# Kernel tuning notes

Measured on AMD Instinct MI355X. Metric: run time of the kernel, lower is better.

## Reference

```python
import jax, jax.numpy as jnp
import numpy as np

EPS = 1e-5  # torch GroupNorm default eps


def _pairwise_sqdist(x, y):
    # squared euclidean distance matrix, clamped at 0 for numerical safety
    d = (jnp.sum(x * x, -1)[:, None] + jnp.sum(y * y, -1)[None, :]
         - 2.0 * (x @ y.T))
    return jnp.maximum(d, 0.0)


def _pc_normalize(ref, src):
    # jointly center and scale both clouds to the unit sphere
    pts = jnp.concatenate([ref, src], axis=0)
    centroid = pts.mean(axis=0, keepdims=True)
    pts = pts - centroid
    m = jnp.max(jnp.linalg.norm(pts, axis=1))
    pts = pts / m
    n_ref = ref.shape[0]
    return pts[:n_ref], pts[n_ref:]


def _group_norm(x, gamma, beta, groups):
    N, C = x.shape
    xg = x.reshape(N, groups, C // groups)
    mean = xg.mean(-1, keepdims=True)
    var = jnp.mean((xg - mean) ** 2, -1, keepdims=True)
    xn = ((xg - mean) / jnp.sqrt(var + EPS)).reshape(N, C)
    return xn * gamma + beta


def setup_inputs() -> dict:
    key = jax.random.key(0)
    ks = jax.random.split(key, 8)
    N_ref, N_src, D = 128, 128, 256
    points_c = jax.random.normal(ks[0], (N_ref + N_src, 3), jnp.float32)
    ref_feats = jax.random.normal(ks[1], (N_ref, D), jnp.float32)
    src_feats = jax.random.normal(ks[2], (N_src, D), jnp.float32)
    # normalized features, as the '_norm' names suggest
    ref_feats = ref_feats / jnp.linalg.norm(ref_feats, axis=-1, keepdims=True)
    src_feats = src_feats / jnp.linalg.norm(src_feats, axis=-1, keepdims=True)
    # a valid rigid transform: random rotation + small translation
    A = jax.random.normal(ks[3], (3, 3), jnp.float32)
    Q, _ = jnp.linalg.qr(A)
    trans = jnp.eye(4, dtype=jnp.float32)
    trans = trans.at[:3, :3].set(Q)
    trans = trans.at[:3, 3].set(jax.random.normal(ks[4], (3,), jnp.float32) * 0.1)
    s = 1.0 / np.sqrt(512)
    return {
        'points_c': points_c,
        'ref_feats_c_norm': ref_feats,
        'src_feats_c_norm': src_feats,
        'trans': trans,
        'W1': jax.random.normal(ks[5], (256, 512), jnp.float32) * s,
        'b1': jnp.zeros((256,), jnp.float32),
        'g1': jnp.ones((256,), jnp.float32),
        'bt1': jnp.zeros((256,), jnp.float32),
        'W2': jax.random.normal(ks[6], (128, 256), jnp.float32) * (1.0 / np.sqrt(256)),
        'b2': jnp.zeros((128,), jnp.float32),
        'g2': jnp.ones((128,), jnp.float32),
        'bt2': jnp.zeros((128,), jnp.float32),
        'W3': jax.random.normal(ks[7], (2, 128), jnp.float32) * (1.0 / np.sqrt(128)),
        'b3': jnp.zeros((2,), jnp.float32),
        'ref_length': 128,
    }


def reference(points_c, ref_feats_c_norm, src_feats_c_norm, trans,
              W1, b1, g1, bt1, W2, b2, g2, bt2, W3, b3, ref_length):
    GROUPS = 8
    ref_points = points_c[:ref_length]
    src_points = points_c[ref_length:]
    # apply rigid transform to src points
    src_points = src_points @ trans[:3, :3].T + trans[:3, 3]
    ref_n, src_n = _pc_normalize(ref_points, src_points)

    dist_mat = jnp.exp(-_pairwise_sqdist(ref_n, src_n))  # [Nr, Ns]
    match_idx_ref = jnp.argmax(dist_mat, axis=1)
    match_idx_src = jnp.argmax(dist_mat, axis=0)
    min_dist_ref = jnp.max(dist_mat, axis=1)
    min_dist_src = jnp.max(dist_mat, axis=0)

    feat_score_mat = ref_feats_c_norm @ src_feats_c_norm.T  # [Nr, Ns]
    feat_match_idx_ref = jnp.argmax(feat_score_mat, axis=1)
    feat_match_idx_src = jnp.argmax(feat_score_mat, axis=0)
    feat_match_ref = jnp.max(feat_score_mat, axis=1)
    feat_match_src = jnp.max(feat_score_mat, axis=0)

    r_idx = jnp.arange(feat_score_mat.shape[0])
    c_idx = jnp.arange(feat_score_mat.shape[1])
    feat_score_ref = feat_score_mat[r_idx, match_idx_ref]
    feat_score_src = feat_score_mat[match_idx_src, c_idx]
    dist_ref = dist_mat[r_idx, feat_match_idx_ref]
    dist_src = dist_mat[feat_match_idx_src, c_idx]

    min_dist = jnp.concatenate([min_dist_ref, min_dist_src])
    feat_score = jnp.concatenate([feat_score_ref, feat_score_src])
    perm_d = jnp.argsort(-min_dist)  # descending sort
    d_m = min_dist[perm_d] * feat_score[perm_d]

    match_feat = jnp.concatenate([feat_match_ref, feat_match_src])
    match_dist = jnp.concatenate([dist_ref, dist_src])
    perm_f = jnp.argsort(-match_feat)
    m_d = match_dist[perm_f] * match_feat[perm_f]

    geo_out = jnp.concatenate([d_m, m_d])[None, :]  # [1, 512]

    h = _group_norm(geo_out @ W1.T + b1, g1, bt1, GROUPS)
    h = jax.nn.relu(h)
    h = _group_norm(h @ W2.T + b2, g2, bt2, GROUPS)
    h = jax.nn.relu(h)
    return h @ W3.T + b3  # [1, num_classes]
```

## Files before the change

kernel.cpp:

```cpp
#include <hip/hip_runtime.h>
#include <math.h>

#define NREF 128
#define NSRC 128
#define DIM  256
#define EPS  1e-5f

__global__ __launch_bounds__(512) void feat_kernel(
    const float* __restrict__ ref_feats,
    const float* __restrict__ src_feats,
    float* __restrict__ feat_mat)
{
    __shared__ __align__(16) float refrow[DIM];
    const int i = blockIdx.x;
    const int t = threadIdx.x;
    if (t < 64) ((float4*)refrow)[t] = ((const float4*)(ref_feats + i * DIM))[t];
    __syncthreads();

    const int w = t >> 6, l = t & 63;
    const float4 r = ((const float4*)refrow)[l];

    for (int m = 0; m < 16; m += 2) {
        const int j0 = w * 16 + m;
        const int j1 = j0 + 1;
        const float4 a0 = ((const float4*)(src_feats + j0 * DIM))[l];
        const float4 a1 = ((const float4*)(src_feats + j1 * DIM))[l];
        float acc0 = a0.x * r.x + a0.y * r.y + a0.z * r.z + a0.w * r.w;
        float acc1 = a1.x * r.x + a1.y * r.y + a1.z * r.z + a1.w * r.w;
        for (int off = 32; off >= 1; off >>= 1) {
            acc0 += __shfl_down(acc0, off);
            acc1 += __shfl_down(acc1, off);
        }
        if (l == 0) {
            feat_mat[i * NSRC + j0] = acc0;
            feat_mat[i * NSRC + j1] = acc1;
        }
    }
}

__global__ __launch_bounds__(1024) void geo_kernel(
    const float* __restrict__ points_c,
    const float* __restrict__ trans,
    const float* __restrict__ feat_mat,
    float* __restrict__ geo_out)
{
    __shared__ float px[256], py[256], pz[256], nsq[256];
    __shared__ float wred[16];
    __shared__ float red[4];
    __shared__ float pvD[1024]; __shared__ int piD[1024];
    __shared__ float pvF[1024]; __shared__ int piF[1024];
    __shared__ float min_dist[256];   __shared__ int match_idx[256];
    __shared__ float match_feat[256]; __shared__ int feat_idx[256];
    __shared__ float feat_score[256], match_dist[256];
    __shared__ int prD[1024]; __shared__ int prF[1024];

    const int t    = threadIdx.x;
    const int wave = t >> 6;
    const int lane = t & 63;

    float x = 0.f, y = 0.f, z = 0.f;
    if (t < 256) {
        x = points_c[3 * t + 0];
        y = points_c[3 * t + 1];
        z = points_c[3 * t + 2];
        if (t >= NREF) {
            float nx = trans[0] * x + trans[1] * y + trans[2]  * z + trans[3];
            float ny = trans[4] * x + trans[5] * y + trans[6]  * z + trans[7];
            float nz = trans[8] * x + trans[9] * y + trans[10] * z + trans[11];
            x = nx; y = ny; z = nz;
        }
        float sx = x, sy = y, sz = z;
        for (int off = 32; off >= 1; off >>= 1) {
            sx += __shfl_down(sx, off);
            sy += __shfl_down(sy, off);
            sz += __shfl_down(sz, off);
        }
        if (lane == 0) {
            wred[wave]     = sx;
            wred[4 + wave] = sy;
            wred[8 + wave] = sz;
        }
    }
    __syncthreads();
    if (t == 0) {
        red[0] = (wred[0] + wred[1] + wred[2] + wred[3]) * (1.0f / 256.0f);
        red[1] = (wred[4] + wred[5] + wred[6] + wred[7]) * (1.0f / 256.0f);
        red[2] = (wred[8] + wred[9] + wred[10] + wred[11]) * (1.0f / 256.0f);
    }
    __syncthreads();

    if (t < 256) {
        x -= red[0]; y -= red[1]; z -= red[2];
        float n = x * x + y * y + z * z;
        float mx = n;
        for (int off = 32; off >= 1; off >>= 1)
            mx = fmaxf(mx, __shfl_down(mx, off));
        if (lane == 0) wred[wave] = mx;
    }
    __syncthreads();
    if (t == 0)
        red[3] = 1.0f / sqrtf(fmaxf(fmaxf(wred[0], wred[1]), fmaxf(wred[2], wred[3])));
    __syncthreads();
    if (t < 256) {
        const float inv = red[3];
        x *= inv; y *= inv; z *= inv;
        px[t] = x; py[t] = y; pz[t] = z;
        nsq[t] = x * x + y * y + z * z;
    }
    __syncthreads();

    {
        const int rc = t & 255, q = t >> 8;
        float bdv = -1.f; int bdi = 0;
        float bfv = -2.f; int bfi = 0;
        if (rc < 128) {
            const int i = rc;
            for (int m = 0; m < 32; ++m) {
                const int j = q * 32 + m;
                float d = nsq[i] + nsq[128 + j]
                        - 2.0f * (px[i] * px[128 + j] + py[i] * py[128 + j] + pz[i] * pz[128 + j]);
                d = fmaxf(d, 0.f);
                const float v = expf(-d);
                if (v > bdv) { bdv = v; bdi = j; }
                const float f = feat_mat[i * NSRC + j];
                if (f > bfv) { bfv = f; bfi = j; }
            }
        } else {
            const int j = rc - 128;
            for (int m = 0; m < 32; ++m) {
                const int i = q * 32 + m;
                float d = nsq[i] + nsq[128 + j]
                        - 2.0f * (px[i] * px[128 + j] + py[i] * py[128 + j] + pz[i] * pz[128 + j]);
                d = fmaxf(d, 0.f);
                const float v = expf(-d);
                if (v > bdv) { bdv = v; bdi = i; }
                const float f = feat_mat[i * NSRC + j];
                if (f > bfv) { bfv = f; bfi = i; }
            }
        }
        pvD[q * 256 + rc] = bdv; piD[q * 256 + rc] = bdi;
        pvF[q * 256 + rc] = bfv; piF[q * 256 + rc] = bfi;
    }
    __syncthreads();

    if (t < 256) {
        float bv = -1.f; int bi = 0;
        for (int q = 0; q < 4; ++q) {
            const float v = pvD[q * 256 + t];
            if (v > bv) { bv = v; bi = piD[q * 256 + t]; }
        }
        min_dist[t] = bv; match_idx[t] = bi;
        float fv = -2.f; int fi = 0;
        for (int q = 0; q < 4; ++q) {
            const float v = pvF[q * 256 + t];
            if (v > fv) { fv = v; fi = piF[q * 256 + t]; }
        }
        match_feat[t] = fv; feat_idx[t] = fi;
    }
    __syncthreads();

    if (t < 256) {
        if (t < NREF) {
            const int i = t;
            feat_score[t] = feat_mat[i * NSRC + match_idx[t]];
            const int j = feat_idx[t];
            float d = nsq[i] + nsq[128 + j]
                    - 2.0f * (px[i] * px[128 + j] + py[i] * py[128 + j] + pz[i] * pz[128 + j]);
            d = fmaxf(d, 0.f);
            match_dist[t] = expf(-d);
        } else {
            const int j = t - 128;
            feat_score[t] = feat_mat[match_idx[t] * NSRC + j];
            const int i = feat_idx[t];
            float d = nsq[i] + nsq[128 + j]
                    - 2.0f * (px[i] * px[128 + j] + py[i] * py[128 + j] + pz[i] * pz[128 + j]);
            d = fmaxf(d, 0.f);
            match_dist[t] = expf(-d);
        }
    }
    __syncthreads();

    {
        const int e = t & 255, q = t >> 8;
        const float v  = min_dist[e];
        const float wv = match_feat[e];
        int r1 = 0, r2 = 0;
        for (int m = 0; m < 64; ++m) {
            const int j = q * 64 + m;
            const float u  = min_dist[j];
            r1 += (u > v) || (u == v && j < e);
            const float uf = match_feat[j];
            r2 += (uf > wv) || (uf == wv && j < e);
        }
        prD[q * 256 + e] = r1;
        prF[q * 256 + e] = r2;
    }
    __syncthreads();
    if (t < 256) {
        const int r  = prD[t] + prD[256 + t] + prD[512 + t] + prD[768 + t];
        geo_out[r] = min_dist[t] * feat_score[t];
        const int rf = prF[t] + prF[256 + t] + prF[512 + t] + prF[768 + t];
        geo_out[256 + rf] = match_dist[t] * match_feat[t];
    }
}

__global__ __launch_bounds__(64) void mlp1_kernel(
    const float* __restrict__ geo,
    const float* __restrict__ W1, const float* __restrict__ b1,
    float* __restrict__ y1)
{
    const int c = blockIdx.x, l = threadIdx.x;
    const float4 ga = ((const float4*)geo)[l];
    const float4 gb = ((const float4*)geo)[64 + l];
    const float4* __restrict__ wrow = (const float4*)(W1 + c * 512);
    const float4 a = wrow[l];
    const float4 b = wrow[64 + l];
    float acc = a.x * ga.x + a.y * ga.y + a.z * ga.z + a.w * ga.w
              + b.x * gb.x + b.y * gb.y + b.z * gb.z + b.w * gb.w;
    acc += __shfl_down(acc, 32);
    acc += __shfl_down(acc, 16);
    acc += __shfl_down(acc, 8);
    acc += __shfl_down(acc, 4);
    acc += __shfl_down(acc, 2);
    acc += __shfl_down(acc, 1);
    if (l == 0) y1[c] = acc + b1[c];
}

__global__ __launch_bounds__(64) void mlp2_kernel(
    const float* __restrict__ y1,
    const float* __restrict__ g1, const float* __restrict__ bt1,
    const float* __restrict__ W2, const float* __restrict__ b2,
    float* __restrict__ y2)
{
    __shared__ __align__(16) float y1s[256];
    __shared__ float stats[16];
    const int c = blockIdx.x, l = threadIdx.x;
    ((float4*)y1s)[l] = ((const float4*)y1)[l];
    __syncthreads();
    if (l < 8) {
        float s = 0.f;
        for (int k = 0; k < 32; ++k) s += y1s[(l << 5) + k];
        const float mean = s * (1.0f / 32.0f);
        float q = 0.f;
        for (int k = 0; k < 32; ++k) { const float d = y1s[(l << 5) + k] - mean; q += d * d; }
        const float var = q * (1.0f / 32.0f);
        stats[l] = mean;
        stats[8 + l] = rsqrtf(var + EPS);
    }
    __syncthreads();
    const float4 gg = ((const float4*)g1)[l];
    const float4 bb = ((const float4*)bt1)[l];
    const int g = l >> 3;
    const float mean = stats[g], inv = stats[8 + g];
    const float4 yv = ((const float4*)y1s)[l];
    float4 h;
    h.x = fmaxf((yv.x - mean) * inv * gg.x + bb.x, 0.f);
    h.y = fmaxf((yv.y - mean) * inv * gg.y + bb.y, 0.f);
    h.z = fmaxf((yv.z - mean) * inv * gg.z + bb.z, 0.f);
    h.w = fmaxf((yv.w - mean) * inv * gg.w + bb.w, 0.f);
    const float4 wv = ((const float4*)(W2 + c * 256))[l];
    float acc = wv.x * h.x + wv.y * h.y + wv.z * h.z + wv.w * h.w;
    acc += __shfl_down(acc, 32);
    acc += __shfl_down(acc, 16);
    acc += __shfl_down(acc, 8);
    acc += __shfl_down(acc, 4);
    acc += __shfl_down(acc, 2);
    acc += __shfl_down(acc, 1);
    if (l == 0) y2[c] = acc + b2[c];
}

__global__ __launch_bounds__(128) void final_kernel(
    const float* __restrict__ y2,
    const float* __restrict__ g2, const float* __restrict__ bt2,
    const float* __restrict__ W3, const float* __restrict__ b3,
    float* __restrict__ out)
{
    __shared__ float y2s[128], h2[128];
    const int t = threadIdx.x;
    y2s[t] = y2[t];
    __syncthreads();
    {
        const int g = t >> 4;
        float s = 0.f;
        for (int k = 0; k < 16; ++k) s += y2s[(g << 4) + k];
        const float mean = s * (1.0f / 16.0f);
        float q = 0.f;
        for (int k = 0; k < 16; ++k) { const float d = y2s[(g << 4) + k] - mean; q += d * d; }
        const float var = q * (1.0f / 16.0f);
        const float xn = (y2s[t] - mean) * rsqrtf(var + EPS);
        h2[t] = fmaxf(xn * g2[t] + bt2[t], 0.f);
    }
    __syncthreads();
    const int wave = t >> 6, lane = t & 63;
    float acc = W3[wave * 128 + lane] * h2[lane]
              + W3[wave * 128 + 64 + lane] * h2[64 + lane];
    acc += __shfl_down(acc, 32);
    acc += __shfl_down(acc, 16);
    acc += __shfl_down(acc, 8);
    acc += __shfl_down(acc, 4);
    acc += __shfl_down(acc, 2);
    acc += __shfl_down(acc, 1);
    if (lane == 0) out[wave] = acc + b3[wave];
}

extern "C" void kernel_launch(void* const* d_in, const int* in_sizes, int n_in,
                              void* d_out, int out_size, void* d_ws, size_t ws_size,
                              hipStream_t stream)
{
    const float* points_c  = (const float*)d_in[0];
    const float* ref_feats = (const float*)d_in[1];
    const float* src_feats = (const float*)d_in[2];
    const float* trans     = (const float*)d_in[3];
    const float* W1  = (const float*)d_in[4];
    const float* b1  = (const float*)d_in[5];
    const float* g1  = (const float*)d_in[6];
    const float* bt1 = (const float*)d_in[7];
    const float* W2  = (const float*)d_in[8];
    const float* b2  = (const float*)d_in[9];
    const float* g2  = (const float*)d_in[10];
    const float* bt2 = (const float*)d_in[11];
    const float* W3  = (const float*)d_in[12];
    const float* b3  = (const float*)d_in[13];

    float* feat_mat = (float*)d_ws;
    float* geo = feat_mat;
    float* y1  = feat_mat + 512;
    float* y2  = feat_mat + 768;

    feat_kernel<<<dim3(NREF), dim3(512), 0, stream>>>(ref_feats, src_feats, feat_mat);
    geo_kernel<<<dim3(1), dim3(1024), 0, stream>>>(points_c, trans, feat_mat, geo);
    mlp1_kernel<<<dim3(256), dim3(64), 0, stream>>>(geo, W1, b1, y1);
    mlp2_kernel<<<dim3(128), dim3(64), 0, stream>>>(y1, g1, bt1, W2, b2, y2);
    final_kernel<<<dim3(1), dim3(128), 0, stream>>>(y2, g2, bt2, W3, b3, (float*)d_out);
}
```

Before: 104.5 us.

## Move point normalization and row feature argmax into feat kernel

An extra block in the feature-similarity kernel now does the point-cloud centering, scaling and squared-norm computation and writes the results to workspace. Each feature row block also computes its own row argmax while producing the dot products. The single-block geo kernel then skips the serial normalization reductions and the row-side feature max scan, reading these precomputed results instead. This shortens the critical path of the one-block kernel, at the cost of extra workspace traffic and an imbalanced extra block in the first kernel.

```diff
diff --git a/kernel.cpp b/kernel.cpp
--- a/kernel.cpp
+++ b/kernel.cpp
@@ -9,16 +9,77 @@
 __global__ __launch_bounds__(512) void feat_kernel(
     const float* __restrict__ ref_feats,
     const float* __restrict__ src_feats,
-    float* __restrict__ feat_mat)
+    const float* __restrict__ points_c,
+    const float* __restrict__ trans,
+    float* __restrict__ feat_mat,
+    float* __restrict__ rowF, int* __restrict__ rowFi,
+    float* __restrict__ pts_ws)
 {
     __shared__ __align__(16) float refrow[DIM];
+    __shared__ float wmv[8];  __shared__ int wmi[8];
+    __shared__ float wred[16], red[4];
+
+    const int t = threadIdx.x;
+    const int w = t >> 6, l = t & 63;
+
+    if (blockIdx.x == 128) {
+        float x = 0.f, y = 0.f, z = 0.f;
+        if (t < 256) {
+            x = points_c[3 * t + 0];
+            y = points_c[3 * t + 1];
+            z = points_c[3 * t + 2];
+            if (t >= NREF) {
+                float nx = trans[0] * x + trans[1] * y + trans[2]  * z + trans[3];
+                float ny = trans[4] * x + trans[5] * y + trans[6]  * z + trans[7];
+                float nz = trans[8] * x + trans[9] * y + trans[10] * z + trans[11];
+                x = nx; y = ny; z = nz;
+            }
+            float sx = x, sy = y, sz = z;
+            for (int off = 32; off >= 1; off >>= 1) {
+                sx += __shfl_down(sx, off);
+                sy += __shfl_down(sy, off);
+                sz += __shfl_down(sz, off);
+            }
+            if (l == 0) {
+                wred[w] = sx; wred[4 + w] = sy; wred[8 + w] = sz;
+            }
+        }
+        __syncthreads();
+        if (t == 0) {
+            red[0] = (wred[0] + wred[1] + wred[2] + wred[3]) * (1.0f / 256.0f);
+            red[1] = (wred[4] + wred[5] + wred[6] + wred[7]) * (1.0f / 256.0f);
+            red[2] = (wred[8] + wred[9] + wred[10] + wred[11]) * (1.0f / 256.0f);
+        }
+        __syncthreads();
+        if (t < 256) {
+            x -= red[0]; y -= red[1]; z -= red[2];
+            float n = x * x + y * y + z * z;
+            float mx = n;
+            for (int off = 32; off >= 1; off >>= 1)
+                mx = fmaxf(mx, __shfl_down(mx, off));
+            if (l == 0) wred[w] = mx;
+        }
+        __syncthreads();
+        if (t == 0)
+            red[3] = 1.0f / sqrtf(fmaxf(fmaxf(wred[0], wred[1]), fmaxf(wred[2], wred[3])));
+        __syncthreads();
+        if (t < 256) {
+            const float inv = red[3];
+            x *= inv; y *= inv; z *= inv;
+            pts_ws[t]       = x;
+            pts_ws[256 + t] = y;
+            pts_ws[512 + t] = z;
+            pts_ws[768 + t] = x * x + y * y + z * z;
+        }
+        return;
+    }
+
     const int i = blockIdx.x;
-    const int t = threadIdx.x;
     if (t < 64) ((float4*)refrow)[t] = ((const float4*)(ref_feats + i * DIM))[t];
     __syncthreads();
 
-    const int w = t >> 6, l = t & 63;
     const float4 r = ((const float4*)refrow)[l];
+    float bv = -2.f; int bi = 0;
 
     for (int m = 0; m < 16; m += 2) {
         const int j0 = w * 16 + m;
@@ -34,87 +95,48 @@
         if (l == 0) {
             feat_mat[i * NSRC + j0] = acc0;
             feat_mat[i * NSRC + j1] = acc1;
-        }
+            if (acc0 > bv) { bv = acc0; bi = j0; }
+            if (acc1 > bv) { bv = acc1; bi = j1; }
+        }
+    }
+    if (l == 0) { wmv[w] = bv; wmi[w] = bi; }
+    __syncthreads();
+    if (t == 0) {
+        float fv = -2.f; int fi = 0;
+        for (int ww = 0; ww < 8; ++ww)
+            if (wmv[ww] > fv) { fv = wmv[ww]; fi = wmi[ww]; }
+        rowF[i] = fv; rowFi[i] = fi;
     }
 }
 
 __global__ __launch_bounds__(1024) void geo_kernel(
-    const float* __restrict__ points_c,
-    const float* __restrict__ trans,
+    const float* __restrict__ pts_ws,
     const float* __restrict__ feat_mat,
+    const float* __restrict__ rowF, const int* __restrict__ rowFi,
     float* __restrict__ geo_out)
 {
     __shared__ float px[256], py[256], pz[256], nsq[256];
-    __shared__ float wred[16];
-    __shared__ float red[4];
     __shared__ float pvD[1024]; __shared__ int piD[1024];
-    __shared__ float pvF[1024]; __shared__ int piF[1024];
+    __shared__ float pvF[512];  __shared__ int piF[512];
     __shared__ float min_dist[256];   __shared__ int match_idx[256];
     __shared__ float match_feat[256]; __shared__ int feat_idx[256];
     __shared__ float feat_score[256], match_dist[256];
     __shared__ int prD[1024]; __shared__ int prF[1024];
 
-    const int t    = threadIdx.x;
-    const int wave = t >> 6;
-    const int lane = t & 63;
-
-    float x = 0.f, y = 0.f, z = 0.f;
+    const int t = threadIdx.x;
     if (t < 256) {
-        x = points_c[3 * t + 0];
-        y = points_c[3 * t + 1];
-        z = points_c[3 * t + 2];
-        if (t >= NREF) {
-            float nx = trans[0] * x + trans[1] * y + trans[2]  * z + trans[3];
-            float ny = trans[4] * x + trans[5] * y + trans[6]  * z + trans[7];
-            float nz = trans[8] * x + trans[9] * y + trans[10] * z + trans[11];
-            x = nx; y = ny; z = nz;
-        }
-        float sx = x, sy = y, sz = z;
-        for (int off = 32; off >= 1; off >>= 1) {
-            sx += __shfl_down(sx, off);
-            sy += __shfl_down(sy, off);
-            sz += __shfl_down(sz, off);
-        }
-        if (lane == 0) {
-            wred[wave]     = sx;
-            wred[4 + wave] = sy;
-            wred[8 + wave] = sz;
-        }
-    }
-    __syncthreads();
-    if (t == 0) {
-        red[0] = (wred[0] + wred[1] + wred[2] + wred[3]) * (1.0f / 256.0f);
-        red[1] = (wred[4] + wred[5] + wred[6] + wred[7]) * (1.0f / 256.0f);
-        red[2] = (wred[8] + wred[9] + wred[10] + wred[11]) * (1.0f / 256.0f);
-    }
-    __syncthreads();
-
-    if (t < 256) {
-        x -= red[0]; y -= red[1]; z -= red[2];
-        float n = x * x + y * y + z * z;
-        float mx = n;
-        for (int off = 32; off >= 1; off >>= 1)
-            mx = fmaxf(mx, __shfl_down(mx, off));
-        if (lane == 0) wred[wave] = mx;
-    }
-    __syncthreads();
-    if (t == 0)
-        red[3] = 1.0f / sqrtf(fmaxf(fmaxf(wred[0], wred[1]), fmaxf(wred[2], wred[3])));
-    __syncthreads();
-    if (t < 256) {
-        const float inv = red[3];
-        x *= inv; y *= inv; z *= inv;
-        px[t] = x; py[t] = y; pz[t] = z;
-        nsq[t] = x * x + y * y + z * z;
+        px[t]  = pts_ws[t];
+        py[t]  = pts_ws[256 + t];
+        pz[t]  = pts_ws[512 + t];
+        nsq[t] = pts_ws[768 + t];
     }
     __syncthreads();
 
     {
         const int rc = t & 255, q = t >> 8;
-        float bdv = -1.f; int bdi = 0;
-        float bfv = -2.f; int bfi = 0;
         if (rc < 128) {
             const int i = rc;
+            float bdv = -1.f; int bdi = 0;
             for (int m = 0; m < 32; ++m) {
                 const int j = q * 32 + m;
                 float d = nsq[i] + nsq[128 + j]
@@ -122,11 +144,12 @@
                 d = fmaxf(d, 0.f);
                 const float v = expf(-d);
                 if (v > bdv) { bdv = v; bdi = j; }
-                const float f = feat_mat[i * NSRC + j];
-                if (f > bfv) { bfv = f; bfi = j; }
-            }
+            }
+            pvD[q * 256 + rc] = bdv; piD[q * 256 + rc] = bdi;
         } else {
             const int j = rc - 128;
+            float bdv = -1.f; int bdi = 0;
+            float bfv = -2.f; int bfi = 0;
             for (int m = 0; m < 32; ++m) {
                 const int i = q * 32 + m;
                 float d = nsq[i] + nsq[128 + j]
@@ -137,9 +160,9 @@
                 const float f = feat_mat[i * NSRC + j];
                 if (f > bfv) { bfv = f; bfi = i; }
             }
-        }
-        pvD[q * 256 + rc] = bdv; piD[q * 256 + rc] = bdi;
-        pvF[q * 256 + rc] = bfv; piF[q * 256 + rc] = bfi;
+            pvD[q * 256 + rc] = bdv; piD[q * 256 + rc] = bdi;
+            pvF[q * 128 + j]  = bfv; piF[q * 128 + j]  = bfi;
+        }
     }
     __syncthreads();
 
@@ -150,12 +173,17 @@
             if (v > bv) { bv = v; bi = piD[q * 256 + t]; }
         }
         min_dist[t] = bv; match_idx[t] = bi;
-        float fv = -2.f; int fi = 0;
-        for (int q = 0; q < 4; ++q) {
-            const float v = pvF[q * 256 + t];
-            if (v > fv) { fv = v; fi = piF[q * 256 + t]; }
-        }
-        match_feat[t] = fv; feat_idx[t] = fi;
+        if (t < 128) {
+            match_feat[t] = rowF[t]; feat_idx[t] = rowFi[t];
+        } else {
+            const int j = t - 128;
+            float fv = -2.f; int fi = 0;
+            for (int q = 0; q < 4; ++q) {
+                const float v = pvF[q * 128 + j];
+                if (v > fv) { fv = v; fi = piF[q * 128 + j]; }
+            }
+            match_feat[t] = fv; feat_idx[t] = fi;
+        }
     }
     __syncthreads();
 
@@ -322,13 +350,18 @@
     const float* W3  = (const float*)d_in[12];
     const float* b3  = (const float*)d_in[13];
 
-    float* feat_mat = (float*)d_ws;
-    float* geo = feat_mat;
-    float* y1  = feat_mat + 512;
-    float* y2  = feat_mat + 768;
-
-    feat_kernel<<<dim3(NREF), dim3(512), 0, stream>>>(ref_feats, src_feats, feat_mat);
-    geo_kernel<<<dim3(1), dim3(1024), 0, stream>>>(points_c, trans, feat_mat, geo);
+    float* base     = (float*)d_ws;
+    float* feat_mat = base;
+    float* rowF     = base + 16384;
+    int*   rowFi    = (int*)(base + 16512);
+    float* pts_ws   = base + 16640;
+    float* geo      = base + 17664;
+    float* y1       = base + 18176;
+    float* y2       = base + 18432;
+
+    feat_kernel<<<dim3(129), dim3(512), 0, stream>>>(
+        ref_feats, src_feats, points_c, trans, feat_mat, rowF, rowFi, pts_ws);
+    geo_kernel<<<dim3(1), dim3(1024), 0, stream>>>(pts_ws, feat_mat, rowF, rowFi, geo);
     mlp1_kernel<<<dim3(256), dim3(64), 0, stream>>>(geo, W1, b1, y1);
     mlp2_kernel<<<dim3(128), dim3(64), 0, stream>>>(y1, g1, bt1, W2, b2, y2);
     final_kernel<<<dim3(1), dim3(128), 0, stream>>>(y2, g2, bt2, W3, b3, (float*)d_out);
```

Result: slower. 107.2 us (+2.6%).
